# Kernel optimization log

Measured on AMD Instinct MI355X. Metric: run time of the kernel, lower is better.

## Reference

```python
import jax, jax.numpy as jnp
import numpy as np

N_FFT = 2048
HOP = 512
SR = 48000
T = 2_880_000  # 60 s stereo @ 48 kHz, multiple of HOP


def _hann(n):
    # torch.hann_window default (periodic=True)
    return (0.5 - 0.5 * jnp.cos(2.0 * jnp.pi * jnp.arange(n) / n)).astype(jnp.float32)


def _stft(x, win):
    # x: [C, T] -> [C, F, bins] complex64 (torch.stft center=True, reflect pad)
    pad = N_FFT // 2
    xp = jnp.pad(x, ((0, 0), (pad, pad)), mode='reflect')
    n_frames = 1 + (xp.shape[-1] - N_FFT) // HOP
    idx = jnp.arange(n_frames)[:, None] * HOP + jnp.arange(N_FFT)[None, :]
    frames = xp[:, idx] * win  # [C, F, N_FFT]
    return jnp.fft.rfft(frames, axis=-1)


def _istft(S, win, length):
    # S: [C, F, bins] -> [C, length]; overlap-add with window-square normalization
    frames = jnp.fft.irfft(S, n=N_FFT, axis=-1) * win  # [C, F, N_FFT]
    nF = frames.shape[1]
    total = (nF - 1) * HOP + N_FFT
    idx = jnp.arange(nF)[:, None] * HOP + jnp.arange(N_FFT)[None, :]
    ola = jnp.zeros((frames.shape[0], total), frames.dtype).at[:, idx].add(frames)
    wsum = jnp.zeros((total,), win.dtype).at[idx].add(jnp.broadcast_to(win ** 2, idx.shape))
    out = ola / jnp.where(wsum > 1e-11, wsum, 1.0)
    pad = N_FFT // 2
    return out[:, pad:pad + length]


def _eq_band(audio, freq, gain_db, q=1.0):
    win = _hann(N_FFT)
    S = _stft(audio, win)  # [C, F, bins]
    bins = S.shape[-1]
    freqs = jnp.linspace(0.0, 24000.0, bins)
    mask = jnp.exp(-((freqs - freq) / (freq / q)) ** 2)  # [bins]
    g_lin = 10.0 ** (gain_db / 20.0)
    S = S * (1.0 + (g_lin - 1.0) * mask)
    return _istft(S, win, audio.shape[-1])


def _compress(audio, threshold, ratio, attack, release, makeup_gain):
    aa = jnp.abs(audio) + 1e-8
    adb = 20.0 * jnp.log10(aa)
    gr = jnp.maximum(adb - threshold, 0.0) * (1.0 - 1.0 / ratio)  # [C, T]
    a_att = 1.0 - jnp.exp(-1.0 / (attack * SR))
    a_rel = 1.0 - jnp.exp(-1.0 / (release * SR))

    def step(prev, g):
        alpha = jnp.where(g > prev, a_att, a_rel)
        new = (1.0 - alpha) * prev + alpha * g
        return new, new

    init = jnp.zeros((audio.shape[0],), audio.dtype)
    _, gs = jax.lax.scan(step, init, gr[:, 1:].T)  # [T-1, C]
    gain_smooth = jnp.concatenate([init[:, None], gs.T], axis=1)  # [C, T]
    gain_lin = 10.0 ** ((-gain_smooth + makeup_gain) / 20.0)
    return jnp.sign(audio) * aa * gain_lin


def setup_inputs() -> dict:
    key = jax.random.key(0)
    audio = 0.1 * jax.random.normal(key, (2, T), dtype=jnp.float32)
    f32 = lambda v: jnp.float32(v)
    return {
        'audio': audio,
        'eq_low_gain': f32(3.0),
        'eq_low_mid_gain': f32(-2.0),
        'eq_high_mid_gain': f32(2.5),
        'eq_high_gain': f32(1.5),
        'comp_threshold': f32(-18.0),
        'comp_ratio': f32(4.0),
        'comp_attack': f32(0.01),
        'comp_release': f32(0.1),
        'comp_makeup_gain': f32(3.0),
        'saturation': f32(1.5),
    }


def reference(audio, eq_low_gain, eq_low_mid_gain, eq_high_mid_gain, eq_high_gain,
              comp_threshold, comp_ratio, comp_attack, comp_release,
              comp_makeup_gain, saturation):
    x = _eq_band(audio, 100.0, eq_low_gain)
    x = _eq_band(x, 500.0, eq_low_mid_gain)
    x = _eq_band(x, 3000.0, eq_high_mid_gain)
    x = _eq_band(x, 10000.0, eq_high_gain)
    x = _compress(x, comp_threshold, comp_ratio, comp_attack, comp_release, comp_makeup_gain)
    # saturation branch (original: python if on .item(); here jnp.where)
    return jnp.where(saturation > 1.0, jnp.tanh(x * saturation) / saturation, x)
```

## Files before the change

### kernel.cpp

```cpp
#include <hip/hip_runtime.h>
#include <math.h>

#define T_LEN   2880000
#define LASTFR  5625
#define NBLK_EQ 1875
#define SEG     7680
#define NSEG    375
#define KREC    15
#define NREC    512
#define PROWS   528
#define RST     384
#define PL      (PROWS * RST)
#define SPL     (NREC * RST)

typedef float2 c2;
__device__ __forceinline__ c2 cadd(c2 a, c2 b){ return make_float2(a.x+b.x, a.y+b.y); }
__device__ __forceinline__ c2 csub(c2 a, c2 b){ return make_float2(a.x-b.x, a.y-b.y); }
__device__ __forceinline__ c2 cmul(c2 a, c2 b){ return make_float2(a.x*b.x - a.y*b.y, a.x*b.y + a.y*b.x); }
__device__ __forceinline__ c2 cmulj(c2 a, c2 b){ return make_float2(a.x*b.x + a.y*b.y, a.y*b.x - a.x*b.y); }

template<int SGN>
__device__ __forceinline__ void dft8(c2 v[8]) {
    const float r = 0.70710678118654752f;
    c2 t0 = cadd(v[0], v[4]), t1 = csub(v[0], v[4]);
    c2 t2 = cadd(v[2], v[6]), t3 = csub(v[2], v[6]);
    c2 u0 = cadd(v[1], v[5]), u1 = csub(v[1], v[5]);
    c2 u2 = cadd(v[3], v[7]), u3 = csub(v[3], v[7]);
    c2 t3r = (SGN < 0) ? make_float2(t3.y, -t3.x) : make_float2(-t3.y, t3.x);
    c2 u3r = (SGN < 0) ? make_float2(u3.y, -u3.x) : make_float2(-u3.y, u3.x);
    c2 E0 = cadd(t0, t2), E2 = csub(t0, t2);
    c2 E1 = cadd(t1, t3r), E3 = csub(t1, t3r);
    c2 O0 = cadd(u0, u2), O2 = csub(u0, u2);
    c2 O1 = cadd(u1, u3r), O3 = csub(u1, u3r);
    c2 O1w = (SGN < 0) ? make_float2(r*(O1.x+O1.y), r*(O1.y-O1.x))
                       : make_float2(r*(O1.x-O1.y), r*(O1.x+O1.y));
    c2 O2w = (SGN < 0) ? make_float2(O2.y, -O2.x) : make_float2(-O2.y, O2.x);
    c2 O3w = (SGN < 0) ? make_float2(r*(O3.y-O3.x), -r*(O3.x+O3.y))
                       : make_float2(-r*(O3.x+O3.y), r*(O3.x-O3.y));
    v[0] = cadd(E0, O0);  v[4] = csub(E0, O0);
    v[1] = cadd(E1, O1w); v[5] = csub(E1, O1w);
    v[2] = cadd(E2, O2w); v[6] = csub(E2, O2w);
    v[3] = cadd(E3, O3w); v[7] = csub(E3, O3w);
}

__device__ __forceinline__ c2 shx(c2 v, int m) {
    return make_float2(__shfl_xor(v.x, m), __shfl_xor(v.y, m));
}

__device__ __forceinline__ void emit_chunk(float* __restrict__ dst, const float* __restrict__ WN,
                                           int cchunk, int tid, c2 r0, c2 r1) {
    const bool edge = (cchunk <= 2) || (cchunk >= 5626);
    #pragma unroll
    for (int q = 0; q < 2; ++q) {
        c2 rr = (q == 0) ? r0 : r1;
        int m = cchunk * 512 + (q << 8) + tid;
        float inv = 0.66666666666667f;
        if (edge) {
            int tmn = (m >= 2048) ? (((m - 2048) >> 9) + 1) : 0;
            int tmx = min(LASTFR, m >> 9);
            float wsum = 0.0f;
            for (int tt = tmn; tt <= tmx; ++tt) {
                float w = WN[m - (tt << 9)];
                wsum += w * w;
            }
            inv = (wsum > 1e-11f) ? (1.0f / wsum) : 1.0f;
        }
        int o = m - 1024;
        dst[o]         = rr.x * inv;
        dst[T_LEN + o] = rr.y * inv;
    }
}

__global__ __launch_bounds__(256) void eq_band_kernel(
    const float* __restrict__ src, float* __restrict__ dst,
    const float* __restrict__ gain_db_p, const float f0)
{
    __shared__ c2 SA[2048];
    __shared__ c2 TWs2[256];
    __shared__ c2 TWs3[32];
    __shared__ float WN[2048];

    const int tid = threadIdx.x;
    const int b   = blockIdx.x;

    const float gdb   = *gain_db_p;
    const float g_lin = exp2f(gdb * 0.16609640474436813f);
    const float gm1   = g_lin - 1.0f;

    const float st2048 = 6.283185307179586f / 2048.0f;
    for (int idx = tid; idx < 2048; idx += 256) {
        WN[idx] = 0.5f - 0.5f * cosf(st2048 * (float)idx);
    }
    {
        int m = tid >> 5, j2 = tid & 31;
        float ang = (6.283185307179586f / 256.0f) * (float)(j2 * m);
        TWs2[tid] = make_float2(cosf(ang), -sinf(ang));
    }
    if (tid < 32) {
        int m = tid >> 2, j = tid & 3;
        float ang = (6.283185307179586f / 32.0f) * (float)(j * m);
        TWs3[tid] = make_float2(cosf(ang), -sinf(ang));
    }

    c2 tw1[8];
    float mk[8];
    tw1[0] = make_float2(1.0f, 0.0f);
    #pragma unroll
    for (int m = 1; m < 8; ++m) {
        float ang = st2048 * (float)(tid * m);
        tw1[m] = make_float2(cosf(ang), -sinf(ang));
    }
    #pragma unroll
    for (int m = 0; m < 8; ++m) {
        int tt = tid;
        int bb = tt >> 2, jj = tt & 3;
        int qrev = ((jj & 1) << 1) | (jj >> 1);
        int k = (bb >> 3) + ((bb & 7) << 3) + (m << 6) + (qrev << 9);
        int kk = (k > 1024) ? (2048 - k) : k;
        float f = (float)kk * (24000.0f / 1024.0f);
        float d = (f - f0) / f0;
        mk[m] = (1.0f + gm1 * expf(-d * d)) * (1.0f / 2048.0f);
    }
    __syncthreads();

    const int t0   = max(0, 3 * b - 1);
    const int t1   = min(LASTFR, 3 * b + 4);
    const int cmin = 3 * b + 2;
    const int cmax = 3 * b + 4;

    c2 ring[8];
    #pragma unroll
    for (int q = 0; q < 8; ++q) ring[q] = make_float2(0.0f, 0.0f);

    for (int t = t0; t <= t1; ++t) {
        for (int j = tid; j < 2048; j += 256) {
            int ss = t * 512 + j - 1024;
            ss = (ss < 0) ? -ss : ss;
            ss = (ss >= T_LEN) ? (2 * T_LEN - 2 - ss) : ss;
            float w = WN[j];
            SA[j] = make_float2(src[ss] * w, src[T_LEN + ss] * w);
        }
        __syncthreads();

        c2 v[8];

        #pragma unroll
        for (int k = 0; k < 8; ++k) v[k] = SA[tid + (k << 8)];
        dft8<-1>(v);
        #pragma unroll
        for (int m = 1; m < 8; ++m) v[m] = cmul(v[m], tw1[m]);
        #pragma unroll
        for (int m = 0; m < 8; ++m) SA[tid + (m << 8)] = v[m];
        __syncthreads();

        {
            int c = tid >> 5, j2 = tid & 31;
            int base = (c << 8) + j2;
            #pragma unroll
            for (int k = 0; k < 8; ++k) v[k] = SA[base + (k << 5)];
            dft8<-1>(v);
            #pragma unroll
            for (int m = 1; m < 8; ++m) v[m] = cmul(v[m], TWs2[(m << 5) + j2]);
            __syncthreads();
            #pragma unroll
            for (int m = 0; m < 8; ++m) SA[(c << 8) + (m << 5) + (j2 ^ (m << 2))] = v[m];
        }
        __syncthreads();

        {
            int bb = tid >> 2, j = tid & 3;
            int base = bb << 5, bx = (bb & 7) << 2;
            #pragma unroll
            for (int k = 0; k < 8; ++k) v[k] = SA[base + ((k << 2) ^ bx) + j];
            dft8<-1>(v);
            #pragma unroll
            for (int m = 1; m < 8; ++m) v[m] = cmul(v[m], TWs3[(m << 2) + j]);
            #pragma unroll
            for (int m = 0; m < 8; ++m) {
                c2 w = v[m];
                c2 p = shx(w, 2);
                c2 e  = (j & 2) ? csub(p, w) : cadd(w, p);
                c2 qq = shx(e, 1);
                c2 lo = (j & 1) ? csub(qq, e) : cadd(e, qq);
                c2 hi = (j & 1) ? make_float2(qq.x - e.y, qq.y + e.x)
                                : make_float2(e.x + qq.y, e.y - qq.x);
                w = (j & 2) ? hi : lo;
                float mkv = mk[m];
                w.x *= mkv; w.y *= mkv;
                c2 p2 = shx(w, 1);
                c2 e2 = (j & 1) ? csub(p2, w) : cadd(w, p2);
                c2 q2 = shx(e2, 2);
                c2 lo2 = (j & 1) ? make_float2(e2.x - q2.y, e2.y + q2.x)
                                 : cadd(e2, q2);
                c2 hi2 = (j & 1) ? make_float2(q2.x + e2.y, q2.y - e2.x)
                                 : csub(q2, e2);
                v[m] = (j & 2) ? hi2 : lo2;
            }
            #pragma unroll
            for (int m = 1; m < 8; ++m) v[m] = cmulj(v[m], TWs3[(m << 2) + j]);
            dft8<+1>(v);
            __syncthreads();
            #pragma unroll
            for (int k = 0; k < 8; ++k) SA[base + ((k << 2) ^ bx) + j] = v[k];
        }
        __syncthreads();

        {
            int c = tid >> 5, j2 = tid & 31;
            #pragma unroll
            for (int m = 0; m < 8; ++m) v[m] = SA[(c << 8) + (m << 5) + (j2 ^ (m << 2))];
            #pragma unroll
            for (int m = 1; m < 8; ++m) v[m] = cmulj(v[m], TWs2[(m << 5) + j2]);
            dft8<+1>(v);
            __syncthreads();
            #pragma unroll
            for (int k = 0; k < 8; ++k) SA[(c << 8) + (k << 5) + j2] = v[k];
        }
        __syncthreads();

        {
            #pragma unroll
            for (int m = 0; m < 8; ++m) v[m] = SA[tid + (m << 8)];
            #pragma unroll
            for (int m = 1; m < 8; ++m) v[m] = cmulj(v[m], tw1[m]);
            dft8<+1>(v);
            #pragma unroll
            for (int k = 0; k < 8; ++k) {
                float w = WN[tid + (k << 8)];
                ring[k].x += v[k].x * w;
                ring[k].y += v[k].y * w;
            }
        }
        __syncthreads();

        if (t >= cmin) emit_chunk(dst, WN, t, tid, ring[0], ring[1]);
        #pragma unroll
        for (int q = 0; q < 6; ++q) ring[q] = ring[q + 2];
        ring[6] = make_float2(0.0f, 0.0f);
        ring[7] = make_float2(0.0f, 0.0f);
    }
    for (int c = t1 + 1; c <= cmax; ++c) {
        emit_chunk(dst, WN, c, tid, ring[0], ring[1]);
        #pragma unroll
        for (int q = 0; q < 6; ++q) ring[q] = ring[q + 2];
        ring[6] = make_float2(0.0f, 0.0f);
        ring[7] = make_float2(0.0f, 0.0f);
    }
}

__device__ __forceinline__ float gaval(float v, float thr, float coef) {
    float aa = fabsf(v) + 1e-8f;
    return fmaxf(6.020599913279624f * __log2f(aa) - thr, 0.0f) * coef;
}

__global__ __launch_bounds__(256) void rec15_kernel(
    const float* __restrict__ y, float4* __restrict__ rec,
    const float* __restrict__ thr_p, const float* __restrict__ ratio_p,
    const float* __restrict__ att_p, const float* __restrict__ rel_p)
{
    __shared__ float4 Lsub[32][9][4];
    const int r0 = blockIdx.x * 32;
    const int s0 = blockIdx.y * 64;
    const int c  = blockIdx.z;
    const int tid = threadIdx.x;

    float thr = *thr_p, ratio = *ratio_p;
    float A  = expf(-1.0f / ((*att_p) * 48000.0f));
    float Bc = expf(-1.0f / ((*rel_p) * 48000.0f));
    float ra = (1.0f - Bc) / (1.0f - A);
    float coef = (1.0f - 1.0f / ratio) * (1.0f - A);

    const int rr = tid & 31, cg = tid >> 5;
    const int orow = tid >> 3, oc8 = tid & 7;

    #pragma unroll 1
    for (int it = 0; it < 8; ++it) {
        int s = s0 + it * 8 + cg;
        if (s < NSEG) {
            int r = r0 + rr;
            int li = s * SEG + KREC * r;
            const float* yp = y + (long)c * T_LEN + li;
            float I[16];
            float a = gaval(yp[0], thr, coef);
            if (li == 0) a = 0.0f;
            I[0] = a; I[1] = ra * a;
            #pragma unroll
            for (int n = 1; n < KREC; ++n) {
                a = gaval(yp[n], thr, coef);
                float b = ra * a;
                I[n + 1] = fmaf(Bc, I[n], b);
                #pragma unroll
                for (int j = n; j >= 1; --j)
                    I[j] = fmaxf(fmaf(A, I[j], a), fmaf(Bc, I[j - 1], b));
                I[0] = fmaf(A, I[0], a);
            }
            Lsub[rr][cg][0] = make_float4(I[0],  I[1],  I[2],  I[3]);
            Lsub[rr][cg][1] = make_float4(I[4],  I[5],  I[6],  I[7]);
            Lsub[rr][cg][2] = make_float4(I[8],  I[9],  I[10], I[11]);
            Lsub[rr][cg][3] = make_float4(I[12], I[13], I[14], I[15]);
        }
        __syncthreads();
        int so = s0 + it * 8 + oc8;
        if (so < NSEG) {
            #pragma unroll
            for (int q = 0; q < 4; ++q)
                rec[(long)(c * 4 + q) * PL + (r0 + orow) * RST + 4 + so]
                    = Lsub[orow][oc8][q];
        }
        __syncthreads();
    }
}


struct Rec { float4 a, b, c, d; };

__device__ __forceinline__ void load8(Rec (&bb)[8],
    const float4* p0, const float4* p1, const float4* p2, const float4* p3, int r)
{
    #pragma unroll
    for (int k = 0; k < 8; ++k) {
        int o = (r + k) * RST;
        bb[k].a = p0[o]; bb[k].b = p1[o]; bb[k].c = p2[o]; bb[k].d = p3[o];
    }
}

template<bool STORE>
__device__ __forceinline__ void consume8(Rec (&bb)[8], float* sp, int r, float& p,
                                         const float (&S)[16])
{
    #pragma unroll
    for (int k = 0; k < 8; ++k) {
        Rec v = bb[k];
        float m0 = fmaxf(fmaf(S[0],  p, v.a.x), fmaf(S[1],  p, v.a.y));
        float m1 = fmaxf(fmaf(S[2],  p, v.a.z), fmaf(S[3],  p, v.a.w));
        float m2 = fmaxf(fmaf(S[4],  p, v.b.x), fmaf(S[5],  p, v.b.y));
        float m3 = fmaxf(fmaf(S[6],  p, v.b.z), fmaf(S[7],  p, v.b.w));
        float m4 = fmaxf(fmaf(S[8],  p, v.c.x), fmaf(S[9],  p, v.c.y));
        float m5 = fmaxf(fmaf(S[10], p, v.c.z), fmaf(S[11], p, v.c.w));
        float m6 = fmaxf(fmaf(S[12], p, v.d.x), fmaf(S[13], p, v.d.y));
        float m7 = fmaxf(fmaf(S[14], p, v.d.z), fmaf(S[15], p, v.d.w));
        m0 = fmaxf(m0, m1); m2 = fmaxf(m2, m3);
        m4 = fmaxf(m4, m5); m6 = fmaxf(m6, m7);
        m0 = fmaxf(m0, m2); m4 = fmaxf(m4, m6);
        p = fmaxf(m0, m4);
        if (STORE) sp[(r + k) * RST] = p;
    }
}

template<bool STORE>
__device__ void scan_pass(const float4* p0, const float4* p1, const float4* p2,
                          const float4* p3, float* sp, float& p, const float (&S)[16])
{
    Rec bA[8], bB[8];
    load8(bA, p0, p1, p2, p3, 0);
    __builtin_amdgcn_sched_barrier(0);
    int r = 0;
    #pragma unroll 1
    for (int gg = 0; gg < NREC / 16; ++gg) {
        load8(bB, p0, p1, p2, p3, r + 8);
        __builtin_amdgcn_sched_barrier(0);
        consume8<STORE>(bA, sp, r, p, S);
        __builtin_amdgcn_sched_barrier(0);
        load8(bA, p0, p1, p2, p3, r + 16);
        __builtin_amdgcn_sched_barrier(0);
        consume8<STORE>(bB, sp, r + 8, p, S);
        __builtin_amdgcn_sched_barrier(0);
        r += 16;
    }
}

template<int MODE>
__global__ __launch_bounds__(64, 1) void scan_iter_kernel(
    const float4* __restrict__ rec, float* __restrict__ gsP,
    const float* __restrict__ eIn, float* __restrict__ eOut,
    const float* __restrict__ att_p, const float* __restrict__ rel_p)
{
    int gid = blockIdx.x * 64 + threadIdx.x;
    int g2 = min(gid, 2 * NSEG - 1);
    int c = g2 / NSEG;
    int s = g2 - c * NSEG;

    float A  = expf(-1.0f / ((*att_p) * 48000.0f));
    float Bc = expf(-1.0f / ((*rel_p) * 48000.0f));
    float S[16];
    {
        float pa = 1.0f;
        #pragma unroll
        for (int j = 15; j >= 0; --j) { S[j] = pa; pa *= A; }
        float pb = 1.0f;
        #pragma unroll
        for (int j = 0; j < 16; ++j) { S[j] *= pb; pb *= Bc; }
    }

    float p = 0.0f;
    if (MODE != 0) p = (s == 0) ? 0.0f : eIn[c * NSEG + s - 1];

    const float4* p0 = rec + (long)(c * 4 + 0) * PL + 4 + s;
    const float4* p1 = rec + (long)(c * 4 + 1) * PL + 4 + s;
    const float4* p2 = rec + (long)(c * 4 + 2) * PL + 4 + s;
    const float4* p3 = rec + (long)(c * 4 + 3) * PL + 4 + s;

    if (MODE == 2) {
        float* sbase = gsP + (long)c * SPL + 4 + s;
        scan_pass<true>(p0, p1, p2, p3, sbase, p, S);
    } else {
        scan_pass<false>(p0, p1, p2, p3, nullptr, p, S);
        eOut[c * NSEG + s] = p;
    }
}

__global__ __launch_bounds__(256) void final_kernel(
    const float* __restrict__ y, const float* __restrict__ gsP, float* __restrict__ out,
    const float* __restrict__ thr_p, const float* __restrict__ ratio_p,
    const float* __restrict__ att_p, const float* __restrict__ rel_p,
    const float* __restrict__ mk_p, const float* __restrict__ sat_p)
{
    __shared__ float LP[64][34];
    const int r0 = blockIdx.x * 32;
    const int s0 = blockIdx.y * 64;
    const int c  = blockIdx.z;
    const int tid = threadIdx.x;

    float thr = *thr_p, ratio = *ratio_p, mk = *mk_p, sat = *sat_p;
    float A  = expf(-1.0f / ((*att_p) * 48000.0f));
    float Bc = expf(-1.0f / ((*rel_p) * 48000.0f));
    float ra = (1.0f - Bc) / (1.0f - A);
    float coef = (1.0f - 1.0f / ratio) * (1.0f - A);
    const float* gb = gsP + (long)c * SPL;

    for (int idx = tid; idx < 33 * 64; idx += 256) {
        int rr = idx >> 6, ss = idx & 63;
        int s = s0 + ss;
        float v = 0.0f;
        if (s < NSEG) {
            int row = r0 - 1 + rr;
            if (row >= 0)      v = gb[row * RST + 4 + s];
            else if (s > 0)    v = gb[(NREC - 1) * RST + 4 + s - 1];
        }
        LP[ss][rr] = v;
    }
    __syncthreads();

    #pragma unroll 1
    for (int it = 0; it < 8; ++it) {
        int idx = it * 256 + tid;
        int ss = idx >> 5, rr = idx & 31;
        int s = s0 + ss;
        if (s >= NSEG) continue;
        int r = r0 + rr;
        int li = s * SEG + KREC * r;
        const float* yp = y + (long)c * T_LEN + li;
        float* op = out + (long)c * T_LEN + li;
        float p = LP[ss][rr];
        #pragma unroll
        for (int q = 0; q < KREC; ++q) {
            float v = yp[q];
            float a = gaval(v, thr, coef);
            if (li + q == 0) a = 0.0f;
            p = fmaxf(fmaf(A, p, a), fmaf(Bc, p, ra * a));
            float aa = fabsf(v) + 1e-8f;
            float gl = exp2f((mk - p) * 0.16609640474436813f);
            float ro = aa * gl;
            ro = (v < 0.0f) ? -ro : ro;
            if (sat > 1.0f) ro = tanhf(ro * sat) / sat;
            op[q] = ro;
        }
    }
}

extern "C" void kernel_launch(void* const* d_in, const int* in_sizes, int n_in,
                              void* d_out, int out_size, void* d_ws, size_t ws_size,
                              hipStream_t stream)
{
    const float* audio = (const float*)d_in[0];
    const float* g1    = (const float*)d_in[1];
    const float* g2    = (const float*)d_in[2];
    const float* g3    = (const float*)d_in[3];
    const float* g4    = (const float*)d_in[4];
    const float* thr   = (const float*)d_in[5];
    const float* ratio = (const float*)d_in[6];
    const float* att   = (const float*)d_in[7];
    const float* rel   = (const float*)d_in[8];
    const float* mkup  = (const float*)d_in[9];
    const float* sat   = (const float*)d_in[10];

    float* out  = (float*)d_out;
    float* bufA = (float*)d_ws;
    float4* rec = (float4*)(bufA + 2 * T_LEN);
    float*  gsP = (float*)(rec + 8 * (long)PL);
    float*  eA  = gsP + 2 * (long)SPL;
    float*  eB  = eA + 2 * NSEG;

    eq_band_kernel<<<NBLK_EQ, 256, 0, stream>>>(audio, out,  g1, 100.0f);
    eq_band_kernel<<<NBLK_EQ, 256, 0, stream>>>(out,   bufA, g2, 500.0f);
    eq_band_kernel<<<NBLK_EQ, 256, 0, stream>>>(bufA,  out,  g3, 3000.0f);
    eq_band_kernel<<<NBLK_EQ, 256, 0, stream>>>(out,   bufA, g4, 10000.0f);

    dim3 tgrid(NREC / 32, (NSEG + 63) / 64, 2);
    rec15_kernel<<<tgrid, 256, 0, stream>>>(bufA, rec, thr, ratio, att, rel);

    scan_iter_kernel<0><<<12, 64, 0, stream>>>(rec, gsP, nullptr, eA, att, rel);
    scan_iter_kernel<1><<<12, 64, 0, stream>>>(rec, gsP, eA, eB, att, rel);
    scan_iter_kernel<1><<<12, 64, 0, stream>>>(rec, gsP, eB, eA, att, rel);
    scan_iter_kernel<1><<<12, 64, 0, stream>>>(rec, gsP, eA, eB, att, rel);
    scan_iter_kernel<2><<<12, 64, 0, stream>>>(rec, gsP, eB, nullptr, att, rel);

    final_kernel<<<tgrid, 256, 0, stream>>>(bufA, gsP, out,
                                            thr, ratio, att, rel, mkup, sat);
}
```

Baseline: 815.0 us.

## Replace recompute-window STFT overlap-add with per-frame atomic accumulation plus normalize pass

Each EQ band previously had every block recompute about six FFT frames to emit three output chunks, which is roughly double the FFT work. Now each block handles two frames exactly once and scatters windowed iFFT output into a global accumulator with float atomicAdd. A separate normalize kernel applies the window-sum scaling and re-zeroes the accumulator. This removes the redundant FFTs but adds atomic traffic, extra global memory round trips and four more kernel launches, and float atomics make summation order nondeterministic.

```diff
diff --git a/kernel.cpp b/kernel.cpp
--- a/kernel.cpp
+++ b/kernel.cpp
@@ -3,7 +3,7 @@
 
 #define T_LEN   2880000
 #define LASTFR  5625
-#define NBLK_EQ 1875
+#define NFR     5626
 #define SEG     7680
 #define NSEG    375
 #define KREC    15
@@ -47,50 +47,23 @@
     return make_float2(__shfl_xor(v.x, m), __shfl_xor(v.y, m));
 }
 
-__device__ __forceinline__ void emit_chunk(float* __restrict__ dst, const float* __restrict__ WN,
-                                           int cchunk, int tid, c2 r0, c2 r1) {
-    const bool edge = (cchunk <= 2) || (cchunk >= 5626);
-    #pragma unroll
-    for (int q = 0; q < 2; ++q) {
-        c2 rr = (q == 0) ? r0 : r1;
-        int m = cchunk * 512 + (q << 8) + tid;
-        float inv = 0.66666666666667f;
-        if (edge) {
-            int tmn = (m >= 2048) ? (((m - 2048) >> 9) + 1) : 0;
-            int tmx = min(LASTFR, m >> 9);
-            float wsum = 0.0f;
-            for (int tt = tmn; tt <= tmx; ++tt) {
-                float w = WN[m - (tt << 9)];
-                wsum += w * w;
-            }
-            inv = (wsum > 1e-11f) ? (1.0f / wsum) : 1.0f;
-        }
-        int o = m - 1024;
-        dst[o]         = rr.x * inv;
-        dst[T_LEN + o] = rr.y * inv;
-    }
-}
-
-__global__ __launch_bounds__(256) void eq_band_kernel(
-    const float* __restrict__ src, float* __restrict__ dst,
+#define NFRB 2
+
+__global__ __launch_bounds__(256) void eq_frame_kernel(
+    const float* __restrict__ src, float* __restrict__ acc,
     const float* __restrict__ gain_db_p, const float f0)
 {
     __shared__ c2 SA[2048];
     __shared__ c2 TWs2[256];
     __shared__ c2 TWs3[32];
-    __shared__ float WN[2048];
 
     const int tid = threadIdx.x;
-    const int b   = blockIdx.x;
 
     const float gdb   = *gain_db_p;
     const float g_lin = exp2f(gdb * 0.16609640474436813f);
     const float gm1   = g_lin - 1.0f;
 
     const float st2048 = 6.283185307179586f / 2048.0f;
-    for (int idx = tid; idx < 2048; idx += 256) {
-        WN[idx] = 0.5f - 0.5f * cosf(st2048 * (float)idx);
-    }
     {
         int m = tid >> 5, j2 = tid & 31;
         float ang = (6.283185307179586f / 256.0f) * (float)(j2 * m);
@@ -102,6 +75,10 @@
         TWs3[tid] = make_float2(cosf(ang), -sinf(ang));
     }
 
+    float wn[8];
+    #pragma unroll
+    for (int k = 0; k < 8; ++k)
+        wn[k] = 0.5f - 0.5f * cosf(st2048 * (float)(tid + (k << 8)));
     c2 tw1[8];
     float mk[8];
     tw1[0] = make_float2(1.0f, 0.0f);
@@ -123,21 +100,17 @@
     }
     __syncthreads();
 
-    const int t0   = max(0, 3 * b - 1);
-    const int t1   = min(LASTFR, 3 * b + 4);
-    const int cmin = 3 * b + 2;
-    const int cmax = 3 * b + 4;
-
-    c2 ring[8];
-    #pragma unroll
-    for (int q = 0; q < 8; ++q) ring[q] = make_float2(0.0f, 0.0f);
-
-    for (int t = t0; t <= t1; ++t) {
-        for (int j = tid; j < 2048; j += 256) {
+    #pragma unroll 1
+    for (int f = 0; f < NFRB; ++f) {
+        const int t = blockIdx.x * NFRB + f;
+
+        #pragma unroll
+        for (int k = 0; k < 8; ++k) {
+            int j = tid + (k << 8);
             int ss = t * 512 + j - 1024;
             ss = (ss < 0) ? -ss : ss;
             ss = (ss >= T_LEN) ? (2 * T_LEN - 2 - ss) : ss;
-            float w = WN[j];
+            float w = wn[k];
             SA[j] = make_float2(src[ss] * w, src[T_LEN + ss] * w);
         }
         __syncthreads();
@@ -224,28 +197,60 @@
             #pragma unroll
             for (int m = 1; m < 8; ++m) v[m] = cmulj(v[m], tw1[m]);
             dft8<+1>(v);
+            __syncthreads();
             #pragma unroll
             for (int k = 0; k < 8; ++k) {
-                float w = WN[tid + (k << 8)];
-                ring[k].x += v[k].x * w;
-                ring[k].y += v[k].y * w;
+                float w = wn[k];
+                int o = t * 512 + (k << 8) + tid - 1024;
+                if (o >= 0 && o < T_LEN) {
+                    atomicAdd(&acc[o],         v[k].x * w);
+                    atomicAdd(&acc[T_LEN + o], v[k].y * w);
+                }
             }
         }
-        __syncthreads();
-
-        if (t >= cmin) emit_chunk(dst, WN, t, tid, ring[0], ring[1]);
-        #pragma unroll
-        for (int q = 0; q < 6; ++q) ring[q] = ring[q + 2];
-        ring[6] = make_float2(0.0f, 0.0f);
-        ring[7] = make_float2(0.0f, 0.0f);
-    }
-    for (int c = t1 + 1; c <= cmax; ++c) {
-        emit_chunk(dst, WN, c, tid, ring[0], ring[1]);
-        #pragma unroll
-        for (int q = 0; q < 6; ++q) ring[q] = ring[q + 2];
-        ring[6] = make_float2(0.0f, 0.0f);
-        ring[7] = make_float2(0.0f, 0.0f);
-    }
+    }
+}
+
+__global__ __launch_bounds__(256) void eq_norm_kernel(
+    float* __restrict__ acc, float* __restrict__ dst)
+{
+    int o0 = (blockIdx.x * 256 + threadIdx.x) * 4;
+    if (o0 >= T_LEN) return;
+    float4 aL = *(const float4*)(acc + o0);
+    float4 aR = *(const float4*)(acc + T_LEN + o0);
+    float vL[4] = {aL.x, aL.y, aL.z, aL.w};
+    float vR[4] = {aR.x, aR.y, aR.z, aR.w};
+    float oL[4], oR[4];
+    #pragma unroll
+    for (int i = 0; i < 4; ++i) {
+        int o = o0 + i;
+        float inv = 0.66666666666667f;
+        if (o < 512 || o >= T_LEN - 512) {
+            int m = o + 1024;
+            int tmn = (m >= 2048) ? (((m - 2048) >> 9) + 1) : 0;
+            int tmx = min(LASTFR, m >> 9);
+            float wsum = 0.0f;
+            for (int tt = tmn; tt <= tmx; ++tt) {
+                int x = m - (tt << 9);
+                float w = 0.5f - 0.5f * cosf((6.283185307179586f / 2048.0f) * (float)x);
+                wsum += w * w;
+            }
+            inv = (wsum > 1e-11f) ? (1.0f / wsum) : 1.0f;
+        }
+        oL[i] = vL[i] * inv;
+        oR[i] = vR[i] * inv;
+    }
+    *(float4*)(dst + o0)          = make_float4(oL[0], oL[1], oL[2], oL[3]);
+    *(float4*)(dst + T_LEN + o0)  = make_float4(oR[0], oR[1], oR[2], oR[3]);
+    float4 z = make_float4(0.f, 0.f, 0.f, 0.f);
+    *(float4*)(acc + o0)         = z;
+    *(float4*)(acc + T_LEN + o0) = z;
+}
+
+__global__ __launch_bounds__(256) void zacc_kernel(float4* __restrict__ acc)
+{
+    int i = blockIdx.x * 256 + threadIdx.x;
+    if (i < 2 * T_LEN / 4) acc[i] = make_float4(0.f, 0.f, 0.f, 0.f);
 }
 
 __device__ __forceinline__ float gaval(float v, float thr, float coef) {
@@ -310,7 +315,6 @@
         __syncthreads();
     }
 }
-
 
 struct Rec { float4 a, b, c, d; };
 
@@ -490,11 +494,21 @@
     float*  gsP = (float*)(rec + 8 * (long)PL);
     float*  eA  = gsP + 2 * (long)SPL;
     float*  eB  = eA + 2 * NSEG;
-
-    eq_band_kernel<<<NBLK_EQ, 256, 0, stream>>>(audio, out,  g1, 100.0f);
-    eq_band_kernel<<<NBLK_EQ, 256, 0, stream>>>(out,   bufA, g2, 500.0f);
-    eq_band_kernel<<<NBLK_EQ, 256, 0, stream>>>(bufA,  out,  g3, 3000.0f);
-    eq_band_kernel<<<NBLK_EQ, 256, 0, stream>>>(out,   bufA, g4, 10000.0f);
+    float*  acc = (float*)rec;
+
+    const int NB_F = NFR / NFRB;
+    const int NB_N = (T_LEN / 4 + 255) / 256;
+
+    zacc_kernel<<<(2 * T_LEN / 4 + 255) / 256, 256, 0, stream>>>((float4*)acc);
+
+    eq_frame_kernel<<<NB_F, 256, 0, stream>>>(audio, acc, g1, 100.0f);
+    eq_norm_kernel<<<NB_N, 256, 0, stream>>>(acc, out);
+    eq_frame_kernel<<<NB_F, 256, 0, stream>>>(out,   acc, g2, 500.0f);
+    eq_norm_kernel<<<NB_N, 256, 0, stream>>>(acc, bufA);
+    eq_frame_kernel<<<NB_F, 256, 0, stream>>>(bufA,  acc, g3, 3000.0f);
+    eq_norm_kernel<<<NB_N, 256, 0, stream>>>(acc, out);
+    eq_frame_kernel<<<NB_F, 256, 0, stream>>>(out,   acc, g4, 10000.0f);
+    eq_norm_kernel<<<NB_N, 256, 0, stream>>>(acc, bufA);
 
     dim3 tgrid(NREC / 32, (NSEG + 63) / 64, 2);
     rec15_kernel<<<tgrid, 256, 0, stream>>>(bufA, rec, thr, ratio, att, rel);
```

After: 771.2 us. 1.06x faster.

## Widen EQ blocks to seven frames and deepen scan load pipeline

Applied to the files above, without the earlier changes.

The EQ kernel now processes seven output frames per block instead of three, cutting the grid from 1875 to 804 blocks. This reduces the redundant overlap frames each block must recompute at its edges. The scan pass swaps its two-stage, 8-record double buffer for a four-slot ring of 4-record buffers, so up to 12 records of loads stay in flight while each group is consumed. The cost is fewer blocks to fill the GPU, more serial work per EQ block, and possible extra register pressure in the scan.

```diff
diff --git a/kernel.cpp b/kernel.cpp
--- a/kernel.cpp
+++ b/kernel.cpp
@@ -3,7 +3,8 @@
 
 #define T_LEN   2880000
 #define LASTFR  5625
-#define NBLK_EQ 1875
+#define CCH     7
+#define NBLK_EQ 804
 #define SEG     7680
 #define NSEG    375
 #define KREC    15
@@ -123,10 +124,10 @@
     }
     __syncthreads();
 
-    const int t0   = max(0, 3 * b - 1);
-    const int t1   = min(LASTFR, 3 * b + 4);
-    const int cmin = 3 * b + 2;
-    const int cmax = 3 * b + 4;
+    const int cmin = CCH * b + 2;
+    const int cmax = min(5626, CCH * b + CCH + 1);
+    const int t0   = max(0, CCH * b - 1);
+    const int t1   = min(LASTFR, cmax);
 
     c2 ring[8];
     #pragma unroll
@@ -314,22 +315,22 @@
 
 struct Rec { float4 a, b, c, d; };
 
-__device__ __forceinline__ void load8(Rec (&bb)[8],
+__device__ __forceinline__ void load4(Rec (&bb)[4],
     const float4* p0, const float4* p1, const float4* p2, const float4* p3, int r)
 {
     #pragma unroll
-    for (int k = 0; k < 8; ++k) {
+    for (int k = 0; k < 4; ++k) {
         int o = (r + k) * RST;
         bb[k].a = p0[o]; bb[k].b = p1[o]; bb[k].c = p2[o]; bb[k].d = p3[o];
     }
 }
 
 template<bool STORE>
-__device__ __forceinline__ void consume8(Rec (&bb)[8], float* sp, int r, float& p,
+__device__ __forceinline__ void consume4(Rec (&bb)[4], float* sp, int r, float& p,
                                          const float (&S)[16])
 {
     #pragma unroll
-    for (int k = 0; k < 8; ++k) {
+    for (int k = 0; k < 4; ++k) {
         Rec v = bb[k];
         float m0 = fmaxf(fmaf(S[0],  p, v.a.x), fmaf(S[1],  p, v.a.y));
         float m1 = fmaxf(fmaf(S[2],  p, v.a.z), fmaf(S[3],  p, v.a.w));
@@ -347,24 +348,29 @@
     }
 }
 
+#define SB __builtin_amdgcn_sched_barrier(0)
+
 template<bool STORE>
 __device__ void scan_pass(const float4* p0, const float4* p1, const float4* p2,
                           const float4* p3, float* sp, float& p, const float (&S)[16])
 {
-    Rec bA[8], bB[8];
-    load8(bA, p0, p1, p2, p3, 0);
-    __builtin_amdgcn_sched_barrier(0);
+    Rec b0[4], b1[4], b2[4], b3[4];
+    load4(b0, p0, p1, p2, p3, 0);
+    load4(b1, p0, p1, p2, p3, 4);
+    load4(b2, p0, p1, p2, p3, 8);
+    load4(b3, p0, p1, p2, p3, 12);
+    SB;
     int r = 0;
     #pragma unroll 1
     for (int gg = 0; gg < NREC / 16; ++gg) {
-        load8(bB, p0, p1, p2, p3, r + 8);
-        __builtin_amdgcn_sched_barrier(0);
-        consume8<STORE>(bA, sp, r, p, S);
-        __builtin_amdgcn_sched_barrier(0);
-        load8(bA, p0, p1, p2, p3, r + 16);
-        __builtin_amdgcn_sched_barrier(0);
-        consume8<STORE>(bB, sp, r + 8, p, S);
-        __builtin_amdgcn_sched_barrier(0);
+        consume4<STORE>(b0, sp, r, p, S);      SB;
+        load4(b0, p0, p1, p2, p3, r + 16);     SB;
+        consume4<STORE>(b1, sp, r + 4, p, S);  SB;
+        load4(b1, p0, p1, p2, p3, r + 20);     SB;
+        consume4<STORE>(b2, sp, r + 8, p, S);  SB;
+        load4(b2, p0, p1, p2, p3, r + 24);     SB;
+        consume4<STORE>(b3, sp, r + 12, p, S); SB;
+        load4(b3, p0, p1, p2, p3, r + 28);     SB;
         r += 16;
     }
 }
```

Measured after the change: 806.7 us. Within noise of the previous version (-1.0%).
